# Kernel tuning notes

Measured on AMD Instinct MI355X. Metric: run time of the kernel, lower is better.

Reference implementation:

```python
import jax, jax.numpy as jnp
import numpy as np

N_TOKENS = 32768
D_MODEL = 1024


def setup_inputs() -> dict:
    key = jax.random.key(0)
    kx, kr, kw1, kb1, kw2, kb2 = jax.random.split(key, 6)
    scale = 1.0 / np.sqrt(D_MODEL)
    x = jax.random.normal(kx, (N_TOKENS, D_MODEL), dtype=jnp.float32)
    # RandomScatterRouter: each token independently routed to one of 2 experts
    route = jax.random.randint(kr, (N_TOKENS,), 0, 2, dtype=jnp.int32)
    W1 = jax.random.normal(kw1, (D_MODEL, D_MODEL), dtype=jnp.float32) * scale
    b1 = jax.random.normal(kb1, (D_MODEL,), dtype=jnp.float32) * scale
    W2 = jax.random.normal(kw2, (D_MODEL, D_MODEL), dtype=jnp.float32) * scale
    b2 = jax.random.normal(kb2, (D_MODEL,), dtype=jnp.float32) * scale
    return {"x": x, "W1": W1, "b1": b1, "W2": W2, "b2": b2, "route": route}


def reference(x, W1, b1, W2, b2, route):
    # Semantics of scatter -> expert linears -> gather(reverse_indice):
    #   out[i] = x[i] @ W_{route[i]} + b_{route[i]}  (original token order restored)
    # jit-friendly form: mask-partition tokens to each expert (m0 + m1 == 1),
    # run the two expert GEMMs on the disjoint partitions, sum to recombine.
    m0 = (route == 0).astype(x.dtype)[:, None]  # [N, 1]
    m1 = 1.0 - m0
    y0 = (x * m0) @ W1 + b1 * m0  # expert-1 output on its tokens, zeros elsewhere
    y1 = (x * m1) @ W2 + b2 * m1  # expert-2 output on its tokens, zeros elsewhere
    return y0 + y1
```

## Files before the change

kernel.cpp:

```cpp
#include <hip/hip_runtime.h>

#define NT 32768
#define DM 1024
#define NTOT (NT + 128)

typedef __bf16 bf16x8 __attribute__((ext_vector_type(8)));
typedef float f32x4 __attribute__((ext_vector_type(4)));

#define GLD16(g, l)                                                            \
  __builtin_amdgcn_global_load_lds(                                            \
      (const __attribute__((address_space(1))) void*)(g),                      \
      (__attribute__((address_space(3))) void*)(l), 16, 0, 0)

__device__ __forceinline__ unsigned short f2bf(float f) {
  unsigned u = __float_as_uint(f);
  u += 0x7fffu + ((u >> 16) & 1u);
  return (unsigned short)(u >> 16);
}

__global__ void wt_k(const float* __restrict__ W1, const float* __restrict__ W2,
                     unsigned short* __restrict__ Wt) {
  const float* __restrict__ W = blockIdx.z ? W2 : W1;
  unsigned short* __restrict__ dst = Wt + (size_t)blockIdx.z * DM * DM;
  __shared__ float tile[32][33];
  int tx = threadIdx.x, ty = threadIdx.y;
  int n0 = blockIdx.x * 32, k0 = blockIdx.y * 32;
#pragma unroll
  for (int i = 0; i < 32; i += 8)
    tile[ty + i][tx] = W[(size_t)(k0 + ty + i) * DM + n0 + tx];
  __syncthreads();
#pragma unroll
  for (int i = 0; i < 32; i += 8)
    dst[(size_t)(n0 + ty + i) * DM + k0 + tx] = f2bf(tile[tx][ty + i]);
}

__global__ __launch_bounds__(1024) void route_k(const int* __restrict__ route,
                                                int* __restrict__ idx,
                                                int* __restrict__ counters) {
  __shared__ int wsum[16];
  const int t = threadIdx.x;
  const int lane = t & 63, wv = t >> 6;
  const int base = t * 32;
  const int4* rp = (const int4*)(route + base);
  unsigned mask = 0;
#pragma unroll
  for (int v = 0; v < 8; ++v) {
    int4 q = rp[v];
    mask |= (unsigned)(q.x == 0) << (v * 4 + 0);
    mask |= (unsigned)(q.y == 0) << (v * 4 + 1);
    mask |= (unsigned)(q.z == 0) << (v * 4 + 2);
    mask |= (unsigned)(q.w == 0) << (v * 4 + 3);
  }
  const int c0 = __popc(mask);
  int s = c0;
#pragma unroll
  for (int d = 1; d < 64; d <<= 1) {
    int v = __shfl_up(s, (unsigned)d, 64);
    if (lane >= d) s += v;
  }
  if (lane == 63) wsum[wv] = s;
  __syncthreads();
  int waveBase = 0, total0 = 0;
#pragma unroll
  for (int w = 0; w < 16; ++w) {
    int v = wsum[w];
    if (w < wv) waveBase += v;
    total0 += v;
  }
  const int ex0 = waveBase + s - c0;
  int slot0 = ex0;
  int slot1 = NTOT - 1 - (base - ex0);
#pragma unroll
  for (int i = 0; i < 32; ++i) {
    int token = base + i;
    if ((mask >> i) & 1) idx[slot0++] = token;
    else                 idx[slot1--] = token;
  }
  if (t == 0) { counters[0] = total0; counters[1] = NT - total0; }
}

__global__ __launch_bounds__(256) void copy_k(const float* __restrict__ x,
                                              const int* __restrict__ idx,
                                              const int* __restrict__ counters,
                                              unsigned short* __restrict__ xp) {
  const int t = threadIdx.x, lane = t & 63, wave = t >> 6;
  const int slot0 = blockIdx.x * 64;
  const int n0 = counters[0];
  for (int row = wave; row < 64; row += 4) {
    int slot = slot0 + row;
    if (slot >= n0 && slot < n0 + 128) continue;
    int tok = idx[slot];
    const float4* src = (const float4*)(x + (size_t)tok * DM);
    bf16x8* dst = (bf16x8*)(xp + (size_t)slot * DM);
#pragma unroll
    for (int p = 0; p < 2; ++p) {
      float4 v0 = src[p * 128 + lane * 2];
      float4 v1 = src[p * 128 + lane * 2 + 1];
      bf16x8 pk;
      pk[0] = (__bf16)v0.x; pk[1] = (__bf16)v0.y;
      pk[2] = (__bf16)v0.z; pk[3] = (__bf16)v0.w;
      pk[4] = (__bf16)v1.x; pk[5] = (__bf16)v1.y;
      pk[6] = (__bf16)v1.z; pk[7] = (__bf16)v1.w;
      dst[p * 64 + lane] = pk;
    }
  }
}

__global__ __launch_bounds__(256, 4) void gemm_k(
    const unsigned short* __restrict__ xp,
    const unsigned short* __restrict__ Wt,
    const float* __restrict__ b1, const float* __restrict__ b2,
    const int* __restrict__ idx, const int* __restrict__ counters,
    float* __restrict__ out) {
  __shared__ unsigned short As[128 * 64];
  __shared__ unsigned short Bs[128 * 64];

  const int t = threadIdx.x;
  const int lane = t & 63, wave = t >> 6;

  const int lin = blockIdx.y * 8 + blockIdx.x;
  const int L = (lin & 7) * 257 + (lin >> 3);
  const int row0 = (L >> 3) * 128;
  const int col0 = (L & 7) * 128;

  const int n0 = counters[0];
  const int expert = (row0 < n0) ? 0 : 1;
  const unsigned short* Wte = Wt + (size_t)expert * DM * DM;
  const float* bias = expert ? b2 : b1;

  const int wr = (wave >> 1) * 64;
  const int wc = (wave & 1) * 64;
  const int lr = lane & 15;

  f32x4 acc[4][4] = {};

  for (int k0 = 0; k0 < DM; k0 += 64) {
#pragma unroll
    for (int p = 0; p < 4; ++p) {
      int q = p * 256 + t;
      int r = q >> 3;
      int c = ((q & 7) ^ (r & 7)) * 8;
      GLD16(xp  + (size_t)(row0 + r) * DM + k0 + c, As + q * 8);
      GLD16(Wte + (size_t)(col0 + r) * DM + k0 + c, Bs + q * 8);
    }
    __syncthreads();
#pragma unroll
    for (int s = 0; s < 2; ++s) {
      const int cb = s * 4 + (lane >> 4);
      bf16x8 af[4], bfr[4];
#pragma unroll
      for (int i = 0; i < 4; ++i) {
        int r = wr + i * 16 + lr;
        af[i] = *(const bf16x8*)&As[(r * 8 + (cb ^ (r & 7))) * 8];
      }
#pragma unroll
      for (int j = 0; j < 4; ++j) {
        int r = wc + j * 16 + lr;
        bfr[j] = *(const bf16x8*)&Bs[(r * 8 + (cb ^ (r & 7))) * 8];
      }
#pragma unroll
      for (int i = 0; i < 4; ++i)
#pragma unroll
        for (int j = 0; j < 4; ++j)
          acc[i][j] = __builtin_amdgcn_mfma_f32_16x16x32_bf16(af[i], bfr[j], acc[i][j], 0, 0, 0);
    }
    __syncthreads();
  }

#pragma unroll
  for (int i = 0; i < 4; ++i) {
#pragma unroll
    for (int reg = 0; reg < 4; ++reg) {
      int gr = row0 + wr + i * 16 + (lane >> 4) * 4 + reg;
      if (gr < n0 || gr >= n0 + 128) {
        int dest = idx[gr];
#pragma unroll
        for (int j = 0; j < 4; ++j) {
          int gc = col0 + wc + j * 16 + (lane & 15);
          out[(size_t)dest * DM + gc] = acc[i][j][reg] + bias[gc];
        }
      }
    }
  }
}

extern "C" void kernel_launch(void* const* d_in, const int* in_sizes, int n_in,
                              void* d_out, int out_size, void* d_ws, size_t ws_size,
                              hipStream_t stream) {
  const float* x   = (const float*)d_in[0];
  const float* W1  = (const float*)d_in[1];
  const float* b1  = (const float*)d_in[2];
  const float* W2  = (const float*)d_in[3];
  const float* b2  = (const float*)d_in[4];
  const int*   route = (const int*)d_in[5];
  float* out = (float*)d_out;

  char* ws = (char*)d_ws;
  unsigned short* xp = (unsigned short*)ws;
  size_t off = (size_t)NTOT * DM * 2;
  unsigned short* Wt = (unsigned short*)(ws + off);
  off += (size_t)2 * DM * DM * 2;
  int* idx = (int*)(ws + off);
  int* counters = idx + NTOT;

  route_k<<<1, 1024, 0, stream>>>(route, idx, counters);
  copy_k<<<NTOT / 64, 256, 0, stream>>>(x, idx, counters, xp);
  wt_k<<<dim3(DM / 32, DM / 32, 2), dim3(32, 8), 0, stream>>>(W1, W2, Wt);
  gemm_k<<<dim3(8, NTOT / 128), 256, 0, stream>>>(xp, Wt, b1, b2, idx, counters, out);
}
```

Baseline: 350.8 us.

## Replace gathered bf16 copy with dense conversion and gather rows inside GEMM loads

The separate gather-and-convert kernel that built a permuted bf16 activation buffer is replaced by a dense, fully coalesced fp32-to-bf16 conversion kernel. The GEMM now computes per-thread row pointers from the routing index table and gathers token rows directly during its global-to-LDS loads. This removes the dependence of the conversion on routing and its scattered reads, at the cost of non-contiguous row accesses in the GEMM A-tile loads. Rows in the padding gap point to token 0 and are still masked at store time.

```diff
diff --git a/kernel.cpp b/kernel.cpp
--- a/kernel.cpp
+++ b/kernel.cpp
@@ -32,6 +32,23 @@
 #pragma unroll
   for (int i = 0; i < 32; i += 8)
     dst[(size_t)(n0 + ty + i) * DM + k0 + tx] = f2bf(tile[tx][ty + i]);
+}
+
+__global__ __launch_bounds__(256) void cvt_k(const float* __restrict__ x,
+                                             unsigned short* __restrict__ xb) {
+  const size_t stride = (size_t)2048 * 256;
+  size_t p = (size_t)blockIdx.x * 256 + threadIdx.x;
+#pragma unroll
+  for (int it = 0; it < 8; ++it, p += stride) {
+    float4 v0 = ((const float4*)x)[2 * p];
+    float4 v1 = ((const float4*)x)[2 * p + 1];
+    bf16x8 pk;
+    pk[0] = (__bf16)v0.x; pk[1] = (__bf16)v0.y;
+    pk[2] = (__bf16)v0.z; pk[3] = (__bf16)v0.w;
+    pk[4] = (__bf16)v1.x; pk[5] = (__bf16)v1.y;
+    pk[6] = (__bf16)v1.z; pk[7] = (__bf16)v1.w;
+    ((bf16x8*)xb)[p] = pk;
+  }
 }
 
 __global__ __launch_bounds__(1024) void route_k(const int* __restrict__ route,
@@ -79,35 +96,8 @@
   if (t == 0) { counters[0] = total0; counters[1] = NT - total0; }
 }
 
-__global__ __launch_bounds__(256) void copy_k(const float* __restrict__ x,
-                                              const int* __restrict__ idx,
-                                              const int* __restrict__ counters,
-                                              unsigned short* __restrict__ xp) {
-  const int t = threadIdx.x, lane = t & 63, wave = t >> 6;
-  const int slot0 = blockIdx.x * 64;
-  const int n0 = counters[0];
-  for (int row = wave; row < 64; row += 4) {
-    int slot = slot0 + row;
-    if (slot >= n0 && slot < n0 + 128) continue;
-    int tok = idx[slot];
-    const float4* src = (const float4*)(x + (size_t)tok * DM);
-    bf16x8* dst = (bf16x8*)(xp + (size_t)slot * DM);
-#pragma unroll
-    for (int p = 0; p < 2; ++p) {
-      float4 v0 = src[p * 128 + lane * 2];
-      float4 v1 = src[p * 128 + lane * 2 + 1];
-      bf16x8 pk;
-      pk[0] = (__bf16)v0.x; pk[1] = (__bf16)v0.y;
-      pk[2] = (__bf16)v0.z; pk[3] = (__bf16)v0.w;
-      pk[4] = (__bf16)v1.x; pk[5] = (__bf16)v1.y;
-      pk[6] = (__bf16)v1.z; pk[7] = (__bf16)v1.w;
-      dst[p * 64 + lane] = pk;
-    }
-  }
-}
-
 __global__ __launch_bounds__(256, 4) void gemm_k(
-    const unsigned short* __restrict__ xp,
+    const unsigned short* __restrict__ xb,
     const unsigned short* __restrict__ Wt,
     const float* __restrict__ b1, const float* __restrict__ b2,
     const int* __restrict__ idx, const int* __restrict__ counters,
@@ -132,16 +122,27 @@
   const int wc = (wave & 1) * 64;
   const int lr = lane & 15;
 
+  const int rsub = t >> 3;
+  const int cA = ((t & 7) ^ (rsub & 7)) * 8;
+  const unsigned short* aSrc[4];
+  const unsigned short* bSrc[4];
+#pragma unroll
+  for (int p = 0; p < 4; ++p) {
+    int gr = row0 + p * 32 + rsub;
+    int tok = idx[gr];
+    if (gr >= n0 && gr < n0 + 128) tok = 0;
+    aSrc[p] = xb + (size_t)tok * DM + cA;
+    bSrc[p] = Wte + (size_t)(col0 + p * 32 + rsub) * DM + cA;
+  }
+
   f32x4 acc[4][4] = {};
 
   for (int k0 = 0; k0 < DM; k0 += 64) {
 #pragma unroll
     for (int p = 0; p < 4; ++p) {
       int q = p * 256 + t;
-      int r = q >> 3;
-      int c = ((q & 7) ^ (r & 7)) * 8;
-      GLD16(xp  + (size_t)(row0 + r) * DM + k0 + c, As + q * 8);
-      GLD16(Wte + (size_t)(col0 + r) * DM + k0 + c, Bs + q * 8);
+      GLD16(aSrc[p] + k0, As + q * 8);
+      GLD16(bSrc[p] + k0, Bs + q * 8);
     }
     __syncthreads();
 #pragma unroll
@@ -196,15 +197,15 @@
   float* out = (float*)d_out;
 
   char* ws = (char*)d_ws;
-  unsigned short* xp = (unsigned short*)ws;
-  size_t off = (size_t)NTOT * DM * 2;
+  unsigned short* xb = (unsigned short*)ws;
+  size_t off = (size_t)NT * DM * 2;
   unsigned short* Wt = (unsigned short*)(ws + off);
   off += (size_t)2 * DM * DM * 2;
   int* idx = (int*)(ws + off);
   int* counters = idx + NTOT;
 
   route_k<<<1, 1024, 0, stream>>>(route, idx, counters);
-  copy_k<<<NTOT / 64, 256, 0, stream>>>(x, idx, counters, xp);
+  cvt_k<<<2048, 256, 0, stream>>>(x, xb);
   wt_k<<<dim3(DM / 32, DM / 32, 2), dim3(32, 8), 0, stream>>>(W1, W2, Wt);
-  gemm_k<<<dim3(8, NTOT / 128), 256, 0, stream>>>(xp, Wt, b1, b2, idx, counters, out);
-}
+  gemm_k<<<dim3(8, NTOT / 128), 256, 0, stream>>>(xb, Wt, b1, b2, idx, counters, out);
+}
```

Measured after the change: 352.6 us. No clear change (+0.5%).
